# Optimization experiments

Measured on AMD Instinct MI355X. Metric: run time of the kernel, lower is better.

## Reference

```python
import jax, jax.numpy as jnp
import numpy as np

N_NODES = 50000

def gcn_conv(x, src, dst, W, b, n_nodes):
    # PyG GCNConv: add self-loops, symmetric normalization D^-1/2 (A+I) D^-1/2, then bias
    loop = jnp.arange(n_nodes)
    s = jnp.concatenate([src, loop])
    d = jnp.concatenate([dst, loop])
    deg = jax.ops.segment_sum(jnp.ones(s.shape[0], x.dtype), d, num_segments=n_nodes)
    dinv = jnp.where(deg > 0, jax.lax.rsqrt(deg), 0.0)
    norm = dinv[s] * dinv[d]                      # [E+N]
    h = x @ W                                      # [N, out]
    msg = h[s] * norm[:, None]                     # gather + scale
    out = jax.ops.segment_sum(msg, d, num_segments=n_nodes)  # scatter-add
    return out + b

def setup_inputs() -> dict:
    key = jax.random.key(0)
    ks = jax.random.split(key, 8)
    x = jax.random.normal(ks[0], (N_NODES, 128), jnp.float32)
    edge_index = jax.random.randint(ks[1], (2, 800000), 0, N_NODES)
    def glorot(k, fan_in, fan_out):
        lim = np.sqrt(6.0 / (fan_in + fan_out)).astype(np.float32)
        return jax.random.uniform(k, (fan_in, fan_out), jnp.float32, -lim, lim)
    return {
        "x": x,
        "edge_index": edge_index,
        "conv_w1": glorot(ks[2], 128, 64), "conv_b1": jnp.zeros((64,), jnp.float32),
        "conv_w2": glorot(ks[3], 64, 64),  "conv_b2": jnp.zeros((64,), jnp.float32),
        "fc_w1": glorot(ks[4], 64, 32),    "fc_b1": jnp.zeros((32,), jnp.float32),
        "fc_w2": glorot(ks[5], 32, 1),     "fc_b2": jnp.zeros((1,), jnp.float32),
    }

def reference(x, edge_index, conv_w1, conv_b1, conv_w2, conv_b2, fc_w1, fc_b1, fc_w2, fc_b2):
    src, dst = edge_index[0], edge_index[1]
    h = jnp.tanh(gcn_conv(x, src, dst, conv_w1, conv_b1, N_NODES))
    h = jnp.tanh(gcn_conv(h, src, dst, conv_w2, conv_b2, N_NODES))
    h = jnp.tanh(h @ fc_w1 + fc_b1)  # dropout is identity at inference
    return h @ fc_w2 + fc_b2          # [N, 1]
```

## Files before the change

kernel.cpp:

```cpp
#include <hip/hip_runtime.h>
#include <math.h>

#define TPB 256
#define NBK_MAX 512
#define CAP 4096
#define FILL_CAP 4096
#define SC_CH 16

typedef short bf16x8 __attribute__((ext_vector_type(8)));
typedef float f32x4 __attribute__((ext_vector_type(4)));

__device__ __forceinline__ unsigned short rne_bf16(float f) {
  unsigned u = __float_as_uint(f);
  return (unsigned short)((u + 0x7fffu + ((u >> 16) & 1u)) >> 16);
}
__device__ __forceinline__ float bf16_f(unsigned short v) {
  return __uint_as_float((unsigned)v << 16);
}
__device__ __forceinline__ float blo(unsigned u) { return __uint_as_float(u << 16); }
__device__ __forceinline__ float bhi(unsigned u) { return __uint_as_float(u & 0xffff0000u); }
__device__ __forceinline__ float ftanh(float x) {
  float xc = fminf(fmaxf(x, -15.f), 15.f);
  float e = __expf(2.f * xc);
  return (e - 1.f) * __builtin_amdgcn_rcpf(e + 1.f);
}

__global__ __launch_bounds__(TPB) void k_init(int* __restrict__ gcur,
                                              unsigned short* __restrict__ hz,
                                              int NBK, int N) {
  int i = blockIdx.x * TPB + threadIdx.x;
  if (i < NBK) gcur[i] = i * CAP;
  if (blockIdx.x == 0 && threadIdx.x < 32)
    ((unsigned*)(hz + ((size_t)N << 6)))[threadIdx.x] = 0;
}

__global__ __launch_bounds__(TPB) void k_bscatter(const int* __restrict__ src,
                                                  const int* __restrict__ dst,
                                                  int* __restrict__ gcur,
                                                  unsigned* __restrict__ e2,
                                                  int E, int NBK) {
  __shared__ int h[NBK_MAX];
  __shared__ int base[NBK_MAX];
  int tid = threadIdx.x, blk = blockIdx.x, G = gridDim.x;
  int chunk = (E + G - 1) / G, lo = blk * chunk, hi = min(E, lo + chunk);
  for (int t0 = lo; t0 < hi; t0 += TPB * SC_CH) {
    int sv[SC_CH], dv[SC_CH];
    for (int b = tid; b < NBK; b += TPB) h[b] = 0;
    __syncthreads();
#pragma unroll
    for (int u = 0; u < SC_CH; ++u) {
      int e = t0 + u * TPB + tid;
      if (e < hi) {
        dv[u] = dst[e];
        sv[u] = src[e];
        atomicAdd(&h[dv[u] >> 7], 1);
      } else {
        dv[u] = -1;
      }
    }
    __syncthreads();
    for (int b = tid; b < NBK; b += TPB) {
      int c = h[b];
      if (c) {
        int o = atomicAdd(&gcur[b], c);
        base[b] = min(o, (b + 1) * CAP - c);
      }
    }
    __syncthreads();
    for (int b = tid; b < NBK; b += TPB) h[b] = 0;
    __syncthreads();
#pragma unroll
    for (int u = 0; u < SC_CH; ++u) {
      if (dv[u] >= 0) {
        int bk = dv[u] >> 7;
        int r = atomicAdd(&h[bk], 1);
        e2[base[bk] + r] = ((unsigned)sv[u] << 7) | (unsigned)(dv[u] & 127);
      }
    }
    __syncthreads();
  }
}

__global__ __launch_bounds__(TPB) void k_build(const unsigned* __restrict__ e2,
                                               const int* __restrict__ gcur,
                                               int* __restrict__ rowptr,
                                               int* __restrict__ rowend,
                                               float* __restrict__ dinv,
                                               int* __restrict__ col, int N) {
  __shared__ int c[128], sc[128], cur[128];
  __shared__ int buf[FILL_CAP];
  int tid = threadIdx.x, b = blockIdx.x;
  int st = b * CAP;
  int en = min(gcur[b], st + FILL_CAP);
  int len = en - st;
  if (tid < 128) c[tid] = 0;
  __syncthreads();
  for (int i = st + tid; i < en; i += TPB) atomicAdd(&c[e2[i] & 127u], 1);
  __syncthreads();
  if (tid < 128) sc[tid] = c[tid];
  __syncthreads();
  for (int o = 1; o < 128; o <<= 1) {
    int v = (tid >= o && tid < 128) ? sc[tid - o] : 0;
    __syncthreads();
    if (tid < 128) sc[tid] += v;
    __syncthreads();
  }
  if (tid < 128) {
    int excl = sc[tid] - c[tid];
    cur[tid] = excl;
    int node = b * 128 + tid;
    if (node < N) {
      rowptr[node] = st + excl;
      rowend[node] = st + excl + c[tid];
      dinv[node] = rsqrtf((float)(c[tid] + 1));
    }
  }
  __syncthreads();
  for (int i = st + tid; i < en; i += TPB) {
    unsigned v = e2[i];
    int p = atomicAdd(&cur[v & 127u], 1);
    buf[p] = (int)(v >> 7);
  }
  __syncthreads();
  for (int i = tid; i < len; i += TPB) col[st + i] = buf[i];
}

template <int K, bool AF32>
__global__ __launch_bounds__(TPB) void k_mm(const void* __restrict__ Ap,
                                            const float* __restrict__ W,
                                            const float* __restrict__ dinv,
                                            unsigned short* __restrict__ Hout, int N) {
  constexpr int P = K + 8;
  __shared__ unsigned short sHi[64 * P];
  __shared__ unsigned short sLo[64 * P];
  int tid = threadIdx.x;
  for (int i = tid; i < K * 64; i += TPB) {
    int k = i >> 6, n = i & 63;
    float w = W[i];
    unsigned short hb = rne_bf16(w);
    sHi[n * P + k] = hb;
    sLo[n * P + k] = rne_bf16(w - bf16_f(hb));
  }
  __syncthreads();
  int wave = tid >> 6, lane = tid & 63;
  int oct = lane >> 4, l15 = lane & 15;
  int base = blockIdx.x * 64 + wave * 16;
  int arow = base + l15;
  if (arow >= N) arow = N - 1;
  f32x4 acc[4] = {};
#pragma unroll
  for (int s = 0; s < K / 32; ++s) {
    bf16x8 ahi, alo;
    if (AF32) {
      const float* ap = (const float*)Ap + (size_t)arow * K + s * 32 + oct * 8;
      float4 f0 = *(const float4*)ap;
      float4 f1 = *(const float4*)(ap + 4);
      float fv[8] = {f0.x, f0.y, f0.z, f0.w, f1.x, f1.y, f1.z, f1.w};
#pragma unroll
      for (int j = 0; j < 8; ++j) {
        unsigned short hb = rne_bf16(fv[j]);
        ahi[j] = (short)hb;
        alo[j] = (short)rne_bf16(fv[j] - bf16_f(hb));
      }
    } else {
      ahi = *(const bf16x8*)((const unsigned short*)Ap + (size_t)arow * K + s * 32 + oct * 8);
    }
#pragma unroll
    for (int t = 0; t < 4; ++t) {
      bf16x8 bh = *(const bf16x8*)(sHi + (t * 16 + l15) * P + s * 32 + oct * 8);
      bf16x8 bl = *(const bf16x8*)(sLo + (t * 16 + l15) * P + s * 32 + oct * 8);
      acc[t] = __builtin_amdgcn_mfma_f32_16x16x32_bf16(ahi, bh, acc[t], 0, 0, 0);
      acc[t] = __builtin_amdgcn_mfma_f32_16x16x32_bf16(ahi, bl, acc[t], 0, 0, 0);
      if (AF32)
        acc[t] = __builtin_amdgcn_mfma_f32_16x16x32_bf16(alo, bh, acc[t], 0, 0, 0);
    }
  }
#pragma unroll
  for (int r = 0; r < 4; ++r) {
    int row = base + oct * 4 + r;
    if (row < N) {
      float dv = dinv[row];
#pragma unroll
      for (int t = 0; t < 4; ++t)
        Hout[(size_t)row * 64 + t * 16 + l15] = rne_bf16(acc[t][r] * dv);
    }
  }
}

__device__ __forceinline__ float2 agg_node(int i, const unsigned short* __restrict__ H,
                                           const int* __restrict__ rowptr,
                                           const int* __restrict__ rowend,
                                           const int* __restrict__ col, int NS) {
  int lane = threadIdx.x & 63;
  int f2 = lane & 31, half = lane >> 5;
  unsigned sf = *(const unsigned*)(H + ((size_t)i << 6) + f2 * 2);
  float ax = (half == 0) ? blo(sf) : 0.f;
  float ay = (half == 0) ? bhi(sf) : 0.f;
  int beg = rowptr[i], end = rowend[i];
  for (int c0 = beg; c0 < end; c0 += 64) {
    int jj = c0 + lane;
    int jc = (jj < end) ? jj : beg;
    int sv = col[jc];
    if (jj >= end) sv = NS;
    int lim = min(64, end - c0);
    for (int t = 0; t < lim; t += 16) {
      unsigned hv[8];
#pragma unroll
      for (int g = 0; g < 8; ++g) {
        int e0 = t + g, e1 = t + 8 + g;
        int s0 = __builtin_amdgcn_readlane(sv, e0);
        int s1 = __builtin_amdgcn_readlane(sv, e1);
        int s = half ? s1 : s0;
        hv[g] = *(const unsigned*)(H + ((size_t)s << 6) + f2 * 2);
      }
#pragma unroll
      for (int g = 0; g < 8; ++g) {
        ax += blo(hv[g]);
        ay += bhi(hv[g]);
      }
    }
  }
  ax += __shfl_xor(ax, 32);
  ay += __shfl_xor(ay, 32);
  return make_float2(ax, ay);
}

template <bool DOFC>
__global__ __launch_bounds__(TPB) void k_agg(const unsigned short* __restrict__ H,
                                             const int* __restrict__ rowptr,
                                             const int* __restrict__ rowend,
                                             const int* __restrict__ col,
                                             const float* __restrict__ dinv,
                                             const float* __restrict__ bias,
                                             unsigned short* __restrict__ OUT,
                                             const float* __restrict__ fw1,
                                             const float* __restrict__ fb1,
                                             const float* __restrict__ fw2,
                                             const float* __restrict__ fb2,
                                             float* __restrict__ fout, int N) {
  int tid = threadIdx.x;
  int wid = tid >> 6, lane = tid & 63;
  int f2 = lane & 31, half = lane >> 5;
  float2 bf = *(const float2*)(bias + f2 * 2);
  if constexpr (!DOFC) {
    int i = (blockIdx.x * TPB + tid) >> 6;
    if (i >= N) return;
    float di = dinv[i];
    float2 v = agg_node(i, H, rowptr, rowend, col, N);
    if (half == 0) {
      unsigned pk = (unsigned)rne_bf16(ftanh(di * v.x + bf.x)) |
                    ((unsigned)rne_bf16(ftanh(di * v.y + bf.y)) << 16);
      ((unsigned*)OUT)[((size_t)i << 5) + f2] = pk;
    }
  } else {
    __shared__ float sw1t[32 * 66];
    __shared__ float sb1[32];
    __shared__ float sw2[32];
    __shared__ float sA[4 * 64];
    for (int i = tid; i < 32 * 64; i += TPB) {
      int j = i >> 6, k = i & 63;
      sw1t[j * 66 + k] = fw1[k * 32 + j];
    }
    if (tid < 32) { sb1[tid] = fb1[tid]; sw2[tid] = fw2[tid]; }
    __syncthreads();
    int ngroups = (N + 3) / 4;
    float b2v = fb2[0];
    for (int grp = blockIdx.x; grp < ngroups; grp += gridDim.x) {
      int i = grp * 4 + wid;
      float2 v = make_float2(0.f, 0.f);
      float di = 0.f;
      if (i < N) {
        di = dinv[i];
        v = agg_node(i, H, rowptr, rowend, col, N);
      }
      if (half == 0) {
        sA[wid * 64 + f2 * 2 + 0] = ftanh(di * v.x + bf.x);
        sA[wid * 64 + f2 * 2 + 1] = ftanh(di * v.y + bf.y);
      }
      __syncthreads();
      if (tid < 128) {
        int n = tid >> 5, j = tid & 31;
        int node = grp * 4 + n;
        if (node < N) {
          float acc = sb1[j];
          const float2* ar = (const float2*)(sA + n * 64);
          const float2* wr = (const float2*)(sw1t + j * 66);
#pragma unroll
          for (int k2 = 0; k2 < 32; ++k2) {
            float2 av = ar[k2];
            float2 wv = wr[k2];
            acc += av.x * wv.x + av.y * wv.y;
          }
          float t = ftanh(acc) * sw2[j];
#pragma unroll
          for (int o = 1; o < 32; o <<= 1) t += __shfl_xor(t, o);
          if (j == 0) fout[node] = t + b2v;
        }
      }
      __syncthreads();
    }
  }
}


extern "C" void kernel_launch(void* const* d_in, const int* in_sizes, int n_in,
                              void* d_out, int out_size, void* d_ws, size_t ws_size,
                              hipStream_t stream) {
  const float* x   = (const float*)d_in[0];
  const int*   ei  = (const int*)d_in[1];
  const float* w1  = (const float*)d_in[2];
  const float* b1  = (const float*)d_in[3];
  const float* w2  = (const float*)d_in[4];
  const float* b2  = (const float*)d_in[5];
  const float* fw1 = (const float*)d_in[6];
  const float* fb1 = (const float*)d_in[7];
  const float* fw2 = (const float*)d_in[8];
  const float* fb2 = (const float*)d_in[9];
  float* out = (float*)d_out;

  int N = in_sizes[0] / 128;
  int E = in_sizes[1] / 2;
  const int* src = ei;
  const int* dst = ei + E;

  const int G   = 256;
  const int NBK = (N + 127) / 128;

  char* p = (char*)d_ws;
  size_t off = 0;
  auto take = [&](size_t bytes) -> void* {
    void* r = p + off;
    off += (bytes + 255) & ~(size_t)255;
    return r;
  };
  int*            gcur   = (int*)take((size_t)NBK * 4);
  int*            rowptr = (int*)take((size_t)N * 4);
  int*            rowend = (int*)take((size_t)N * 4);
  float*          dinv   = (float*)take((size_t)N * 4);
  unsigned*       e2     = (unsigned*)take((size_t)NBK * CAP * 4);
  int*            col    = (int*)take((size_t)NBK * CAP * 4);
  unsigned short* h      = (unsigned short*)take((size_t)(N + 1) * 64 * 2);
  unsigned short* a      = (unsigned short*)take((size_t)N * 64 * 2);
  (void)ws_size; (void)n_in; (void)out_size;

  k_init<<<(NBK + TPB - 1) / TPB, TPB, 0, stream>>>(gcur, h, NBK, N);
  k_bscatter<<<G, TPB, 0, stream>>>(src, dst, gcur, e2, E, NBK);
  k_build<<<NBK, TPB, 0, stream>>>(e2, gcur, rowptr, rowend, dinv, col, N);

  int gmm = (N + 63) / 64;
  k_mm<128, true><<<gmm, TPB, 0, stream>>>(x, w1, dinv, h, N);
  k_agg<false><<<(N + 3) / 4, TPB, 0, stream>>>(h, rowptr, rowend, col, dinv, b1, a,
                                                nullptr, nullptr, nullptr, nullptr,
                                                nullptr, N);
  k_mm<64, false><<<gmm, TPB, 0, stream>>>(a, w2, dinv, h, N);
  k_agg<true><<<4096, TPB, 0, stream>>>(h, rowptr, rowend, col, dinv, b2, nullptr,
                                        fw1, fb1, fw2, fb2, out, N);
}
```

Measured before the change: 191.3 us.

## Fuse layer-1 aggregation with layer-2 matmul and aggregate two nodes per wave

The second GEMM is folded into the first aggregation kernel. Each wave aggregates a pair of nodes, applies tanh, then multiplies by W2, which it holds in registers, using readlane broadcasts. This removes one kernel launch and the round trip of the intermediate activation through global memory. The gather now uses one bf16 lane per feature with two nodes interleaved for more memory-level parallelism. In exchange, register pressure rises from the 64-float W2 copy, and the second matmul now runs in fp32 scalar FMA instead of MFMA.

```diff
diff --git a/kernel.cpp b/kernel.cpp
--- a/kernel.cpp
+++ b/kernel.cpp
@@ -17,8 +17,9 @@
 __device__ __forceinline__ float bf16_f(unsigned short v) {
   return __uint_as_float((unsigned)v << 16);
 }
-__device__ __forceinline__ float blo(unsigned u) { return __uint_as_float(u << 16); }
-__device__ __forceinline__ float bhi(unsigned u) { return __uint_as_float(u & 0xffff0000u); }
+__device__ __forceinline__ float rl_f(float v, int l) {
+  return __int_as_float(__builtin_amdgcn_readlane(__float_as_int(v), l));
+}
 __device__ __forceinline__ float ftanh(float x) {
   float xc = fminf(fmaxf(x, -15.f), 15.f);
   float e = __expf(2.f * xc);
@@ -26,12 +27,17 @@
 }
 
 __global__ __launch_bounds__(TPB) void k_init(int* __restrict__ gcur,
-                                              unsigned short* __restrict__ hz,
+                                              unsigned short* __restrict__ h1z,
+                                              unsigned short* __restrict__ h2z,
                                               int NBK, int N) {
   int i = blockIdx.x * TPB + threadIdx.x;
   if (i < NBK) gcur[i] = i * CAP;
-  if (blockIdx.x == 0 && threadIdx.x < 32)
-    ((unsigned*)(hz + ((size_t)N << 6)))[threadIdx.x] = 0;
+  if (blockIdx.x == 0) {
+    if (threadIdx.x < 32)
+      ((unsigned*)(h1z + ((size_t)N << 6)))[threadIdx.x] = 0;
+    else if (threadIdx.x < 64)
+      ((unsigned*)(h2z + ((size_t)N << 6)))[threadIdx.x - 32] = 0;
+  }
 }
 
 __global__ __launch_bounds__(TPB) void k_bscatter(const int* __restrict__ src,
@@ -125,8 +131,8 @@
   for (int i = tid; i < len; i += TPB) col[st + i] = buf[i];
 }
 
-template <int K, bool AF32>
-__global__ __launch_bounds__(TPB) void k_mm(const void* __restrict__ Ap,
+template <int K>
+__global__ __launch_bounds__(TPB) void k_mm(const float* __restrict__ Ap,
                                             const float* __restrict__ W,
                                             const float* __restrict__ dinv,
                                             unsigned short* __restrict__ Hout, int N) {
@@ -151,19 +157,15 @@
 #pragma unroll
   for (int s = 0; s < K / 32; ++s) {
     bf16x8 ahi, alo;
-    if (AF32) {
-      const float* ap = (const float*)Ap + (size_t)arow * K + s * 32 + oct * 8;
-      float4 f0 = *(const float4*)ap;
-      float4 f1 = *(const float4*)(ap + 4);
-      float fv[8] = {f0.x, f0.y, f0.z, f0.w, f1.x, f1.y, f1.z, f1.w};
-#pragma unroll
-      for (int j = 0; j < 8; ++j) {
-        unsigned short hb = rne_bf16(fv[j]);
-        ahi[j] = (short)hb;
-        alo[j] = (short)rne_bf16(fv[j] - bf16_f(hb));
-      }
-    } else {
-      ahi = *(const bf16x8*)((const unsigned short*)Ap + (size_t)arow * K + s * 32 + oct * 8);
+    const float* ap = Ap + (size_t)arow * K + s * 32 + oct * 8;
+    float4 f0 = *(const float4*)ap;
+    float4 f1 = *(const float4*)(ap + 4);
+    float fv[8] = {f0.x, f0.y, f0.z, f0.w, f1.x, f1.y, f1.z, f1.w};
+#pragma unroll
+    for (int j = 0; j < 8; ++j) {
+      unsigned short hb = rne_bf16(fv[j]);
+      ahi[j] = (short)hb;
+      alo[j] = (short)rne_bf16(fv[j] - bf16_f(hb));
     }
 #pragma unroll
     for (int t = 0; t < 4; ++t) {
@@ -171,8 +173,7 @@
       bf16x8 bl = *(const bf16x8*)(sLo + (t * 16 + l15) * P + s * 32 + oct * 8);
       acc[t] = __builtin_amdgcn_mfma_f32_16x16x32_bf16(ahi, bh, acc[t], 0, 0, 0);
       acc[t] = __builtin_amdgcn_mfma_f32_16x16x32_bf16(ahi, bl, acc[t], 0, 0, 0);
-      if (AF32)
-        acc[t] = __builtin_amdgcn_mfma_f32_16x16x32_bf16(alo, bh, acc[t], 0, 0, 0);
+      acc[t] = __builtin_amdgcn_mfma_f32_16x16x32_bf16(alo, bh, acc[t], 0, 0, 0);
     }
   }
 #pragma unroll
@@ -187,118 +188,180 @@
   }
 }
 
-__device__ __forceinline__ float2 agg_node(int i, const unsigned short* __restrict__ H,
-                                           const int* __restrict__ rowptr,
-                                           const int* __restrict__ rowend,
-                                           const int* __restrict__ col, int NS) {
+__device__ __forceinline__ void agg_pair(int i0, int i1,
+                                         const unsigned short* __restrict__ H,
+                                         const int* __restrict__ rowptr,
+                                         const int* __restrict__ rowend,
+                                         const int* __restrict__ col, int NS,
+                                         float& o0, float& o1) {
   int lane = threadIdx.x & 63;
-  int f2 = lane & 31, half = lane >> 5;
-  unsigned sf = *(const unsigned*)(H + ((size_t)i << 6) + f2 * 2);
-  float ax = (half == 0) ? blo(sf) : 0.f;
-  float ay = (half == 0) ? bhi(sf) : 0.f;
-  int beg = rowptr[i], end = rowend[i];
-  for (int c0 = beg; c0 < end; c0 += 64) {
+  float a0 = bf16_f(H[((size_t)i0 << 6) + lane]);
+  float a1 = bf16_f(H[((size_t)i1 << 6) + lane]);
+  int b0 = rowptr[i0], e0 = rowend[i0];
+  int b1 = rowptr[i1], e1 = rowend[i1];
+  int jj0 = b0 + lane, jj1 = b1 + lane;
+  int sv0 = col[(jj0 < e0) ? jj0 : b0];
+  if (jj0 >= e0) sv0 = NS;
+  int sv1 = col[(jj1 < e1) ? jj1 : b1];
+  if (jj1 >= e1) sv1 = NS;
+  int l0 = e0 - b0, l1 = e1 - b1;
+  int lm = max(l0, l1);
+  if (lm > 64) lm = 64;
+  for (int t = 0; t < lm; t += 8) {
+    int s0 = __builtin_amdgcn_readlane(sv0, t + 0);
+    int s1 = __builtin_amdgcn_readlane(sv0, t + 1);
+    int s2 = __builtin_amdgcn_readlane(sv0, t + 2);
+    int s3 = __builtin_amdgcn_readlane(sv0, t + 3);
+    int s4 = __builtin_amdgcn_readlane(sv0, t + 4);
+    int s5 = __builtin_amdgcn_readlane(sv0, t + 5);
+    int s6 = __builtin_amdgcn_readlane(sv0, t + 6);
+    int s7 = __builtin_amdgcn_readlane(sv0, t + 7);
+    int u0 = __builtin_amdgcn_readlane(sv1, t + 0);
+    int u1 = __builtin_amdgcn_readlane(sv1, t + 1);
+    int u2 = __builtin_amdgcn_readlane(sv1, t + 2);
+    int u3 = __builtin_amdgcn_readlane(sv1, t + 3);
+    int u4 = __builtin_amdgcn_readlane(sv1, t + 4);
+    int u5 = __builtin_amdgcn_readlane(sv1, t + 5);
+    int u6 = __builtin_amdgcn_readlane(sv1, t + 6);
+    int u7 = __builtin_amdgcn_readlane(sv1, t + 7);
+    unsigned short g0 = H[((size_t)s0 << 6) + lane];
+    unsigned short g1 = H[((size_t)s1 << 6) + lane];
+    unsigned short g2 = H[((size_t)s2 << 6) + lane];
+    unsigned short g3 = H[((size_t)s3 << 6) + lane];
+    unsigned short g4 = H[((size_t)s4 << 6) + lane];
+    unsigned short g5 = H[((size_t)s5 << 6) + lane];
+    unsigned short g6 = H[((size_t)s6 << 6) + lane];
+    unsigned short g7 = H[((size_t)s7 << 6) + lane];
+    unsigned short q0 = H[((size_t)u0 << 6) + lane];
+    unsigned short q1 = H[((size_t)u1 << 6) + lane];
+    unsigned short q2 = H[((size_t)u2 << 6) + lane];
+    unsigned short q3 = H[((size_t)u3 << 6) + lane];
+    unsigned short q4 = H[((size_t)u4 << 6) + lane];
+    unsigned short q5 = H[((size_t)u5 << 6) + lane];
+    unsigned short q6 = H[((size_t)u6 << 6) + lane];
+    unsigned short q7 = H[((size_t)u7 << 6) + lane];
+    a0 += bf16_f(g0); a0 += bf16_f(g1); a0 += bf16_f(g2); a0 += bf16_f(g3);
+    a0 += bf16_f(g4); a0 += bf16_f(g5); a0 += bf16_f(g6); a0 += bf16_f(g7);
+    a1 += bf16_f(q0); a1 += bf16_f(q1); a1 += bf16_f(q2); a1 += bf16_f(q3);
+    a1 += bf16_f(q4); a1 += bf16_f(q5); a1 += bf16_f(q6); a1 += bf16_f(q7);
+  }
+  for (int c0 = b0 + 64; c0 < e0; c0 += 64) {
     int jj = c0 + lane;
-    int jc = (jj < end) ? jj : beg;
-    int sv = col[jc];
-    if (jj >= end) sv = NS;
-    int lim = min(64, end - c0);
-    for (int t = 0; t < lim; t += 16) {
-      unsigned hv[8];
-#pragma unroll
-      for (int g = 0; g < 8; ++g) {
-        int e0 = t + g, e1 = t + 8 + g;
-        int s0 = __builtin_amdgcn_readlane(sv, e0);
-        int s1 = __builtin_amdgcn_readlane(sv, e1);
-        int s = half ? s1 : s0;
-        hv[g] = *(const unsigned*)(H + ((size_t)s << 6) + f2 * 2);
+    int sv = col[(jj < e0) ? jj : b0];
+    if (jj >= e0) sv = NS;
+    int lim = min(64, e0 - c0);
+    for (int t = 0; t < lim; ++t) {
+      int s = __builtin_amdgcn_readlane(sv, t);
+      a0 += bf16_f(H[((size_t)s << 6) + lane]);
+    }
+  }
+  for (int c0 = b1 + 64; c0 < e1; c0 += 64) {
+    int jj = c0 + lane;
+    int sv = col[(jj < e1) ? jj : b1];
+    if (jj >= e1) sv = NS;
+    int lim = min(64, e1 - c0);
+    for (int t = 0; t < lim; ++t) {
+      int s = __builtin_amdgcn_readlane(sv, t);
+      a1 += bf16_f(H[((size_t)s << 6) + lane]);
+    }
+  }
+  o0 = a0;
+  o1 = a1;
+}
+
+__global__ __launch_bounds__(TPB, 4) void k_aggmm(const unsigned short* __restrict__ H1,
+                                                  const int* __restrict__ rowptr,
+                                                  const int* __restrict__ rowend,
+                                                  const int* __restrict__ col,
+                                                  const float* __restrict__ dinv,
+                                                  const float* __restrict__ bias,
+                                                  const float* __restrict__ W2,
+                                                  unsigned short* __restrict__ H2, int N) {
+  __shared__ float w2s[64 * 64];
+  int tid = threadIdx.x;
+  for (int i = tid; i < 64 * 64; i += TPB) w2s[i] = W2[i];
+  __syncthreads();
+  int lane = tid & 63, wid = tid >> 6;
+  float w2r[64];
+#pragma unroll
+  for (int k = 0; k < 64; ++k) w2r[k] = w2s[k * 64 + lane];
+  float bfeat = bias[lane];
+  int gw = gridDim.x * 4;
+  int npairs = (N + 1) / 2;
+  for (int p = blockIdx.x * 4 + wid; p < npairs; p += gw) {
+    int i0 = 2 * p;
+    int i1 = min(2 * p + 1, N - 1);
+    float v0, v1;
+    agg_pair(i0, i1, H1, rowptr, rowend, col, N, v0, v1);
+    float t0 = ftanh(dinv[i0] * v0 + bfeat);
+    float t1 = ftanh(dinv[i1] * v1 + bfeat);
+    float m0 = 0.f, m1 = 0.f;
+#pragma unroll
+    for (int k = 0; k < 64; ++k) {
+      m0 += rl_f(t0, k) * w2r[k];
+      m1 += rl_f(t1, k) * w2r[k];
+    }
+    H2[((size_t)i0 << 6) + lane] = rne_bf16(m0 * dinv[i0]);
+    if (i1 != i0)
+      H2[((size_t)i1 << 6) + lane] = rne_bf16(m1 * dinv[i1]);
+  }
+}
+
+__global__ __launch_bounds__(TPB) void k_aggfc(const unsigned short* __restrict__ H2,
+                                               const int* __restrict__ rowptr,
+                                               const int* __restrict__ rowend,
+                                               const int* __restrict__ col,
+                                               const float* __restrict__ dinv,
+                                               const float* __restrict__ bias,
+                                               const float* __restrict__ fw1,
+                                               const float* __restrict__ fb1,
+                                               const float* __restrict__ fw2,
+                                               const float* __restrict__ fb2,
+                                               float* __restrict__ fout, int N) {
+  __shared__ float sw1t[32 * 66];
+  __shared__ float sb1[32];
+  __shared__ float sw2[32];
+  __shared__ float sA[8 * 64];
+  int tid = threadIdx.x;
+  for (int i = tid; i < 32 * 64; i += TPB) {
+    int j = i >> 6, k = i & 63;
+    sw1t[j * 66 + k] = fw1[k * 32 + j];
+  }
+  if (tid < 32) { sb1[tid] = fb1[tid]; sw2[tid] = fw2[tid]; }
+  __syncthreads();
+  int wid = tid >> 6, lane = tid & 63;
+  float bfeat = bias[lane];
+  float b2v = fb2[0];
+  int ngroups = (N + 7) / 8;
+  for (int grp = blockIdx.x; grp < ngroups; grp += gridDim.x) {
+    int base = grp * 8;
+    int i0 = min(base + wid * 2, N - 1);
+    int i1 = min(base + wid * 2 + 1, N - 1);
+    float v0, v1;
+    agg_pair(i0, i1, H2, rowptr, rowend, col, N, v0, v1);
+    sA[(wid * 2 + 0) * 64 + lane] = ftanh(dinv[i0] * v0 + bfeat);
+    sA[(wid * 2 + 1) * 64 + lane] = ftanh(dinv[i1] * v1 + bfeat);
+    __syncthreads();
+    {
+      int n = tid >> 5, j = tid & 31;
+      int node = base + n;
+      if (node < N) {
+        float acc = sb1[j];
+        const float2* ar = (const float2*)(sA + n * 64);
+        const float2* wr = (const float2*)(sw1t + j * 66);
+#pragma unroll
+        for (int k2 = 0; k2 < 32; ++k2) {
+          float2 av = ar[k2];
+          float2 wv = wr[k2];
+          acc += av.x * wv.x + av.y * wv.y;
+        }
+        float t = ftanh(acc) * sw2[j];
+#pragma unroll
+        for (int o = 1; o < 32; o <<= 1) t += __shfl_xor(t, o);
+        if (j == 0) fout[node] = t + b2v;
       }
-#pragma unroll
-      for (int g = 0; g < 8; ++g) {
-        ax += blo(hv[g]);
-        ay += bhi(hv[g]);
-      }
-    }
-  }
-  ax += __shfl_xor(ax, 32);
-  ay += __shfl_xor(ay, 32);
-  return make_float2(ax, ay);
-}
-
-template <bool DOFC>
-__global__ __launch_bounds__(TPB) void k_agg(const unsigned short* __restrict__ H,
-                                             const int* __restrict__ rowptr,
-                                             const int* __restrict__ rowend,
-                                             const int* __restrict__ col,
-                                             const float* __restrict__ dinv,
-                                             const float* __restrict__ bias,
-                                             unsigned short* __restrict__ OUT,
-                                             const float* __restrict__ fw1,
-                                             const float* __restrict__ fb1,
-                                             const float* __restrict__ fw2,
-                                             const float* __restrict__ fb2,
-                                             float* __restrict__ fout, int N) {
-  int tid = threadIdx.x;
-  int wid = tid >> 6, lane = tid & 63;
-  int f2 = lane & 31, half = lane >> 5;
-  float2 bf = *(const float2*)(bias + f2 * 2);
-  if constexpr (!DOFC) {
-    int i = (blockIdx.x * TPB + tid) >> 6;
-    if (i >= N) return;
-    float di = dinv[i];
-    float2 v = agg_node(i, H, rowptr, rowend, col, N);
-    if (half == 0) {
-      unsigned pk = (unsigned)rne_bf16(ftanh(di * v.x + bf.x)) |
-                    ((unsigned)rne_bf16(ftanh(di * v.y + bf.y)) << 16);
-      ((unsigned*)OUT)[((size_t)i << 5) + f2] = pk;
-    }
-  } else {
-    __shared__ float sw1t[32 * 66];
-    __shared__ float sb1[32];
-    __shared__ float sw2[32];
-    __shared__ float sA[4 * 64];
-    for (int i = tid; i < 32 * 64; i += TPB) {
-      int j = i >> 6, k = i & 63;
-      sw1t[j * 66 + k] = fw1[k * 32 + j];
-    }
-    if (tid < 32) { sb1[tid] = fb1[tid]; sw2[tid] = fw2[tid]; }
-    __syncthreads();
-    int ngroups = (N + 3) / 4;
-    float b2v = fb2[0];
-    for (int grp = blockIdx.x; grp < ngroups; grp += gridDim.x) {
-      int i = grp * 4 + wid;
-      float2 v = make_float2(0.f, 0.f);
-      float di = 0.f;
-      if (i < N) {
-        di = dinv[i];
-        v = agg_node(i, H, rowptr, rowend, col, N);
-      }
-      if (half == 0) {
-        sA[wid * 64 + f2 * 2 + 0] = ftanh(di * v.x + bf.x);
-        sA[wid * 64 + f2 * 2 + 1] = ftanh(di * v.y + bf.y);
-      }
-      __syncthreads();
-      if (tid < 128) {
-        int n = tid >> 5, j = tid & 31;
-        int node = grp * 4 + n;
-        if (node < N) {
-          float acc = sb1[j];
-          const float2* ar = (const float2*)(sA + n * 64);
-          const float2* wr = (const float2*)(sw1t + j * 66);
-#pragma unroll
-          for (int k2 = 0; k2 < 32; ++k2) {
-            float2 av = ar[k2];
-            float2 wv = wr[k2];
-            acc += av.x * wv.x + av.y * wv.y;
-          }
-          float t = ftanh(acc) * sw2[j];
-#pragma unroll
-          for (int o = 1; o < 32; o <<= 1) t += __shfl_xor(t, o);
-          if (j == 0) fout[node] = t + b2v;
-        }
-      }
-      __syncthreads();
-    }
+    }
+    __syncthreads();
   }
 }
 
@@ -338,21 +401,18 @@
   int*            rowend = (int*)take((size_t)N * 4);
   float*          dinv   = (float*)take((size_t)N * 4);
   unsigned*       e2     = (unsigned*)take((size_t)NBK * CAP * 4);
-  int*            col    = (int*)take((size_t)NBK * CAP * 4);
-  unsigned short* h      = (unsigned short*)take((size_t)(N + 1) * 64 * 2);
-  unsigned short* a      = (unsigned short*)take((size_t)N * 64 * 2);
+  int*            col    = (int*)take(((size_t)NBK * CAP + 64) * 4);
+  unsigned short* h1     = (unsigned short*)take((size_t)(N + 1) * 64 * 2);
+  unsigned short* h2     = (unsigned short*)take((size_t)(N + 1) * 64 * 2);
   (void)ws_size; (void)n_in; (void)out_size;
 
-  k_init<<<(NBK + TPB - 1) / TPB, TPB, 0, stream>>>(gcur, h, NBK, N);
+  k_init<<<(NBK + TPB - 1) / TPB, TPB, 0, stream>>>(gcur, h1, h2, NBK, N);
   k_bscatter<<<G, TPB, 0, stream>>>(src, dst, gcur, e2, E, NBK);
   k_build<<<NBK, TPB, 0, stream>>>(e2, gcur, rowptr, rowend, dinv, col, N);
 
   int gmm = (N + 63) / 64;
-  k_mm<128, true><<<gmm, TPB, 0, stream>>>(x, w1, dinv, h, N);
-  k_agg<false><<<(N + 3) / 4, TPB, 0, stream>>>(h, rowptr, rowend, col, dinv, b1, a,
-                                                nullptr, nullptr, nullptr, nullptr,
-                                                nullptr, N);
-  k_mm<64, false><<<gmm, TPB, 0, stream>>>(a, w2, dinv, h, N);
-  k_agg<true><<<4096, TPB, 0, stream>>>(h, rowptr, rowend, col, dinv, b2, nullptr,
-                                        fw1, fb1, fw2, fb2, out, N);
-}
+  k_mm<128><<<gmm, TPB, 0, stream>>>(x, w1, dinv, h1, N);
+  k_aggmm<<<2048, TPB, 0, stream>>>(h1, rowptr, rowend, col, dinv, b1, w2, h2, N);
+  k_aggfc<<<3125, TPB, 0, stream>>>(h2, rowptr, rowend, col, dinv, b2,
+                                    fw1, fb1, fw2, fb2, out, N);
+}
```

Result: no change. 194.4 us (+1.6%).
